# Kernel tuning notes

Hardware: AMD Instinct MI355X
Metric: run time of the kernel (lower is better)

## Reference

```python
import jax, jax.numpy as jnp
import numpy as np

# perm_inv_n with comps = [
#   [[0],[0]]        -> einsum 'Zab->Zb'            (row-sum, prepro eliminates single axis-a)
#   [[0,0],[0,1]]    -> einsum 'Zab,Zac->Zbc'       (Gram matrix over axis a)
#   [[0,0],[0,0]]    -> einsum 'Zab,Zab->Zb'        (column sum of squares)
#   [[0,1],[0,0]]    -> prepro 'Zab->Zb' twice, then 'Zb,Zb->Zb' (squared column sums)
#   [[0,0,1],[0,1,2]]-> prepro arg2 'Zab->Zd', then 'Zab,Zac,Zd->Zbcd' (Gram x colsum outer)
# ] and sz=[512,64]. Outputs are flattened per-Z and concatenated (order = comps order).

def setup_inputs() -> dict:
    key = jax.random.key(0)
    x = jax.random.normal(key, (256, 512, 64), dtype=jnp.float32)
    return {"x": x}

def reference(x) -> jnp.ndarray:
    Z = x.shape[0]
    cs = jnp.sum(x, axis=1)                       # [Z, b]   'Zab->Zb'
    gram = jnp.einsum('zab,zac->zbc', x, x)       # [Z, b, b]
    h1 = cs                                       # comp 0
    h2 = gram.reshape(Z, -1)                      # comp 1
    h3 = jnp.einsum('zab,zab->zb', x, x)          # comp 2
    h4 = cs * cs                                  # comp 3
    h5 = (gram[:, :, :, None] * cs[:, None, None, :]).reshape(Z, -1)  # comp 4: 'Zbc,Zd->Zbcd'
    return jnp.concatenate([h1, h2, h3, h4, h5], axis=-1)  # [Z, 64+4096+64+64+262144]
```

## Files before the change

kernel.cpp:

```cpp
#include <hip/hip_runtime.h>

#define Z_DIM 256
#define A_DIM 512
#define B_DIM 64
#define PER_Z 266432
#define GRAM_OFF 64
#define H3_OFF 4160
#define H4_OFF 4224
#define H5_OFF 4288
#define CHUNK 128

typedef float f4v __attribute__((ext_vector_type(4)));

__global__ __launch_bounds__(512) void k_stats(const float* __restrict__ x,
                                               float* __restrict__ out) {
    __shared__ float sx[2][CHUNK * B_DIM];
    __shared__ float sg[B_DIM * B_DIM];
    __shared__ float scs1[B_DIM];

    const int z = blockIdx.x;
    const int t = threadIdx.x;
    const int half = t >> 8;
    const int u = t & 255;
    const int tb = u >> 4;
    const int tc = u & 15;

    const float* xz = x + (size_t)z * (A_DIM * B_DIM);
    float* oz = out + (size_t)z * PER_Z;

    float acc[4][4];
#pragma unroll
    for (int i = 0; i < 4; i++)
#pragma unroll
        for (int j = 0; j < 4; j++) acc[i][j] = 0.f;
    float cs_acc = 0.f;

    float* my_sx = sx[half];

    for (int c = 0; c < 2; c++) {
        const int a0 = (c * 2 + half) * CHUNK;
        const float4* src = (const float4*)(xz + a0 * B_DIM);
        float4* dst = (float4*)my_sx;
#pragma unroll
        for (int i = 0; i < 8; i++) dst[u + i * 256] = src[u + i * 256];
        __syncthreads();

        for (int a = 0; a < CHUNK; a++) {
            float4 bv = *(const float4*)&my_sx[a * B_DIM + tb * 4];
            float4 cv = *(const float4*)&my_sx[a * B_DIM + tc * 4];
            float bb[4] = {bv.x, bv.y, bv.z, bv.w};
            float cc[4] = {cv.x, cv.y, cv.z, cv.w};
#pragma unroll
            for (int i = 0; i < 4; i++)
#pragma unroll
                for (int j = 0; j < 4; j++)
                    acc[i][j] = fmaf(bb[i], cc[j], acc[i][j]);
        }
        if (u < B_DIM) {
#pragma unroll 4
            for (int a = 0; a < CHUNK; a++) cs_acc += my_sx[a * B_DIM + u];
        }
        __syncthreads();
    }

    if (half) {
#pragma unroll
        for (int i = 0; i < 4; i++) {
            float4 v = make_float4(acc[i][0], acc[i][1], acc[i][2], acc[i][3]);
            *(float4*)&sg[(tb * 4 + i) * B_DIM + tc * 4] = v;
        }
        if (u < B_DIM) scs1[u] = cs_acc;
    }
    __syncthreads();
    if (!half) {
#pragma unroll
        for (int i = 0; i < 4; i++) {
            float4 p = *(const float4*)&sg[(tb * 4 + i) * B_DIM + tc * 4];
            float vv[4] = {acc[i][0] + p.x, acc[i][1] + p.y,
                           acc[i][2] + p.z, acc[i][3] + p.w};
            *(float4*)&oz[GRAM_OFF + (size_t)(tb * 4 + i) * B_DIM + tc * 4] =
                make_float4(vv[0], vv[1], vv[2], vv[3]);
            if (tb == tc) oz[H3_OFF + tb * 4 + i] = vv[i];
        }
        if (u < B_DIM) {
            float c = cs_acc + scs1[u];
            oz[u] = c;
            oz[H4_OFF + u] = c * c;
        }
    }
}

__global__ __launch_bounds__(256) void k_h5(const float* __restrict__ outc,
                                            float* __restrict__ out) {
    __shared__ __align__(16) float sgr[256];
    __shared__ __align__(16) float scs[B_DIM];

    const int z = blockIdx.x >> 4;
    const int s = blockIdx.x & 15;
    const int t = threadIdx.x;

    const float* oz = outc + (size_t)z * PER_Z;
    sgr[t] = oz[GRAM_OFF + s * 256 + t];
    if (t < B_DIM) scs[t] = oz[t];
    __syncthreads();

    const int dg = t & 15;
    const int bq = t >> 4;
    const f4v c4 = *(const f4v*)&scs[dg * 4];

    f4v* o5 = (f4v*)(out + (size_t)z * PER_Z + H5_OFF);
    const size_t base = (size_t)s * 4096 + bq * 16 + dg;
#pragma unroll
    for (int i = 0; i < 16; i++) {
        const float g = sgr[bq + i * 16];
        f4v v = {g * c4.x, g * c4.y, g * c4.z, g * c4.w};
        o5[base + (size_t)i * 256] = v;
    }
}

extern "C" void kernel_launch(void* const* d_in, const int* in_sizes, int n_in,
                              void* d_out, int out_size, void* d_ws, size_t ws_size,
                              hipStream_t stream) {
    const float* x = (const float*)d_in[0];
    float* out = (float*)d_out;
    k_stats<<<Z_DIM, 512, 0, stream>>>(x, out);
    k_h5<<<Z_DIM * 16, 256, 0, stream>>>(out, out);
}
```

Baseline: 314.2 us.

## Use 8x8 per-thread Gram tiles with per-wave K-split and double-buffered loads

Restructures the Gram stats kernel so each wave owns a slice of the a-axis and each lane computes an 8x8 output tile, raising the FMA-to-LDS-load ratio. Global loads of the next 64-row chunk are prefetched into registers while the current chunk is computed (double-buffered LDS), and column sums are taken from the already-loaded values. Partial Gram tiles from 8 waves are combined through a tree reduction in shared memory. Register pressure rises sharply (64 accumulators plus prefetch registers), and the reduction adds several block barriers.

```diff
diff --git a/kernel.cpp b/kernel.cpp
--- a/kernel.cpp
+++ b/kernel.cpp
@@ -8,85 +8,145 @@
 #define H3_OFF 4160
 #define H4_OFF 4224
 #define H5_OFF 4288
-#define CHUNK 128
 
 typedef float f4v __attribute__((ext_vector_type(4)));
 
+__device__ __forceinline__ void wave_store_tile(float* area, const float acc[8][8],
+                                                int R, int C) {
+#pragma unroll
+    for (int i = 0; i < 8; i++) {
+        *(float4*)&area[(R + i) * B_DIM + C] =
+            make_float4(acc[i][0], acc[i][1], acc[i][2], acc[i][3]);
+        *(float4*)&area[(R + i) * B_DIM + C + 4] =
+            make_float4(acc[i][4], acc[i][5], acc[i][6], acc[i][7]);
+    }
+}
+
+__device__ __forceinline__ void wave_add_tile(const float* area, float acc[8][8],
+                                              int R, int C) {
+#pragma unroll
+    for (int i = 0; i < 8; i++) {
+        float4 p0 = *(const float4*)&area[(R + i) * B_DIM + C];
+        float4 p1 = *(const float4*)&area[(R + i) * B_DIM + C + 4];
+        acc[i][0] += p0.x; acc[i][1] += p0.y; acc[i][2] += p0.z; acc[i][3] += p0.w;
+        acc[i][4] += p1.x; acc[i][5] += p1.y; acc[i][6] += p1.z; acc[i][7] += p1.w;
+    }
+}
+
 __global__ __launch_bounds__(512) void k_stats(const float* __restrict__ x,
                                                float* __restrict__ out) {
-    __shared__ float sx[2][CHUNK * B_DIM];
-    __shared__ float sg[B_DIM * B_DIM];
-    __shared__ float scs1[B_DIM];
+    __shared__ float sx[2][B_DIM * B_DIM];
+    __shared__ float csred[8][B_DIM];
 
     const int z = blockIdx.x;
     const int t = threadIdx.x;
-    const int half = t >> 8;
-    const int u = t & 255;
-    const int tb = u >> 4;
-    const int tc = u & 15;
+    const int w = t >> 6;
+    const int l = t & 63;
+    const int R = (l >> 3) * 8;
+    const int C = (l & 7) * 8;
 
     const float* xz = x + (size_t)z * (A_DIM * B_DIM);
     float* oz = out + (size_t)z * PER_Z;
 
-    float acc[4][4];
+    float acc[8][8];
 #pragma unroll
-    for (int i = 0; i < 4; i++)
+    for (int i = 0; i < 8; i++)
 #pragma unroll
-        for (int j = 0; j < 4; j++) acc[i][j] = 0.f;
-    float cs_acc = 0.f;
+        for (int j = 0; j < 8; j++) acc[i][j] = 0.f;
+    float csa[8];
+#pragma unroll
+    for (int j = 0; j < 8; j++) csa[j] = 0.f;
 
-    float* my_sx = sx[half];
+    {
+        const float4* src = (const float4*)xz;
+        float4 r0 = src[t], r1 = src[t + 512];
+        ((float4*)sx[0])[t] = r0;
+        ((float4*)sx[0])[t + 512] = r1;
+    }
+    __syncthreads();
 
-    for (int c = 0; c < 2; c++) {
-        const int a0 = (c * 2 + half) * CHUNK;
-        const float4* src = (const float4*)(xz + a0 * B_DIM);
-        float4* dst = (float4*)my_sx;
+    for (int c = 0; c < 8; ++c) {
+        const float* buf = sx[c & 1];
+        float4 n0, n1;
+        if (c < 7) {
+            const float4* src = (const float4*)(xz + (size_t)(c + 1) * 64 * B_DIM);
+            n0 = src[t];
+            n1 = src[t + 512];
+        }
+        const float* rbase = buf + (w * 8) * B_DIM;
 #pragma unroll
-        for (int i = 0; i < 8; i++) dst[u + i * 256] = src[u + i * 256];
-        __syncthreads();
-
-        for (int a = 0; a < CHUNK; a++) {
-            float4 bv = *(const float4*)&my_sx[a * B_DIM + tb * 4];
-            float4 cv = *(const float4*)&my_sx[a * B_DIM + tc * 4];
-            float bb[4] = {bv.x, bv.y, bv.z, bv.w};
-            float cc[4] = {cv.x, cv.y, cv.z, cv.w};
+        for (int k = 0; k < 8; ++k) {
+            const float* row = rbase + k * B_DIM;
+            float4 b0 = *(const float4*)(row + R);
+            float4 b1 = *(const float4*)(row + R + 4);
+            float4 c0 = *(const float4*)(row + C);
+            float4 c1 = *(const float4*)(row + C + 4);
+            float xb[8] = {b0.x, b0.y, b0.z, b0.w, b1.x, b1.y, b1.z, b1.w};
+            float xc[8] = {c0.x, c0.y, c0.z, c0.w, c1.x, c1.y, c1.z, c1.w};
 #pragma unroll
-            for (int i = 0; i < 4; i++)
+            for (int i = 0; i < 8; i++)
 #pragma unroll
-                for (int j = 0; j < 4; j++)
-                    acc[i][j] = fmaf(bb[i], cc[j], acc[i][j]);
+                for (int j = 0; j < 8; j++)
+                    acc[i][j] = fmaf(xb[i], xc[j], acc[i][j]);
+            if (l < 8) {
+#pragma unroll
+                for (int j = 0; j < 8; j++) csa[j] += xc[j];
+            }
         }
-        if (u < B_DIM) {
-#pragma unroll 4
-            for (int a = 0; a < CHUNK; a++) cs_acc += my_sx[a * B_DIM + u];
+        if (c < 7) {
+            float* nb = sx[(c + 1) & 1];
+            ((float4*)nb)[t] = n0;
+            ((float4*)nb)[t + 512] = n1;
         }
         __syncthreads();
     }
 
-    if (half) {
+    if (l < 8) {
 #pragma unroll
-        for (int i = 0; i < 4; i++) {
-            float4 v = make_float4(acc[i][0], acc[i][1], acc[i][2], acc[i][3]);
-            *(float4*)&sg[(tb * 4 + i) * B_DIM + tc * 4] = v;
+        for (int j = 0; j < 8; j++) csred[w][l * 8 + j] = csa[j];
+    }
+
+    float* area0 = sx[0];
+    float* area1 = sx[1];
+    if (w == 4) wave_store_tile(area0, acc, R, C);
+    if (w == 5) wave_store_tile(area1, acc, R, C);
+    __syncthreads();
+    if (w == 0) wave_add_tile(area0, acc, R, C);
+    if (w == 1) wave_add_tile(area1, acc, R, C);
+    __syncthreads();
+    if (w == 6) wave_store_tile(area0, acc, R, C);
+    if (w == 7) wave_store_tile(area1, acc, R, C);
+    __syncthreads();
+    if (w == 2) wave_add_tile(area0, acc, R, C);
+    if (w == 3) wave_add_tile(area1, acc, R, C);
+    __syncthreads();
+    if (w == 2) wave_store_tile(area0, acc, R, C);
+    if (w == 3) wave_store_tile(area1, acc, R, C);
+    __syncthreads();
+    if (w == 0) wave_add_tile(area0, acc, R, C);
+    if (w == 1) wave_add_tile(area1, acc, R, C);
+    __syncthreads();
+    if (w == 1) wave_store_tile(area0, acc, R, C);
+    __syncthreads();
+
+    if (w == 0) {
+        wave_add_tile(area0, acc, R, C);
+#pragma unroll
+        for (int i = 0; i < 8; i++) {
+            *(float4*)&oz[GRAM_OFF + (size_t)(R + i) * B_DIM + C] =
+                make_float4(acc[i][0], acc[i][1], acc[i][2], acc[i][3]);
+            *(float4*)&oz[GRAM_OFF + (size_t)(R + i) * B_DIM + C + 4] =
+                make_float4(acc[i][4], acc[i][5], acc[i][6], acc[i][7]);
         }
-        if (u < B_DIM) scs1[u] = cs_acc;
-    }
-    __syncthreads();
-    if (!half) {
+        if ((l >> 3) == (l & 7)) {
 #pragma unroll
-        for (int i = 0; i < 4; i++) {
-            float4 p = *(const float4*)&sg[(tb * 4 + i) * B_DIM + tc * 4];
-            float vv[4] = {acc[i][0] + p.x, acc[i][1] + p.y,
-                           acc[i][2] + p.z, acc[i][3] + p.w};
-            *(float4*)&oz[GRAM_OFF + (size_t)(tb * 4 + i) * B_DIM + tc * 4] =
-                make_float4(vv[0], vv[1], vv[2], vv[3]);
-            if (tb == tc) oz[H3_OFF + tb * 4 + i] = vv[i];
+            for (int i = 0; i < 8; i++) oz[H3_OFF + R + i] = acc[i][i];
         }
-        if (u < B_DIM) {
-            float c = cs_acc + scs1[u];
-            oz[u] = c;
-            oz[H4_OFF + u] = c * c;
-        }
+        float cs = 0.f;
+#pragma unroll
+        for (int ww = 0; ww < 8; ww++) cs += csred[ww][l];
+        oz[l] = cs;
+        oz[H4_OFF + l] = cs * cs;
     }
 }
 
```

Result: no change. 308.6 us (median of 2 runs) (-1.8%).
